# Kernel optimization log

Measured on AMD Instinct MI355X. Metric: run time of the kernel, lower is better.

Reference implementation:

```python
import jax, jax.numpy as jnp
import numpy as np


def setup_inputs() -> dict:
    key = jax.random.key(0)
    ks = jax.random.split(key, 8)
    B, Q, K, F, FV, C = 8, 2048, 2048, 512, 512, 2
    q = jax.random.normal(ks[0], (B, Q, F), dtype=jnp.float32)
    k = jax.random.normal(ks[1], (B, K, F), dtype=jnp.float32)
    v = jax.random.normal(ks[2], (B, K, FV), dtype=jnp.float32)
    coords_q = jax.random.uniform(ks[3], (B, Q, C), dtype=jnp.float32)
    coords_k = jax.random.uniform(ks[4], (B, K, C), dtype=jnp.float32)
    attn_mask = jax.random.randint(ks[5], (B, Q, K), 0, 2).astype(bool)
    alibi_mask = jax.random.randint(ks[6], (B, Q, K), 0, 2).astype(bool)
    bias_scale = jax.random.uniform(ks[7], (1,), dtype=jnp.float32)
    return {"q": q, "k": k, "v": v, "coords_q": coords_q, "coords_k": coords_k,
            "attn_mask": attn_mask, "alibi_mask": alibi_mask, "bias_scale": bias_scale}


def reference(q, k, v, coords_q, coords_k, attn_mask, alibi_mask, bias_scale):
    # scaled dot-product logits: [B, Q, K]
    scale = k.shape[-1] ** -0.5
    weight_logits = jnp.einsum('bqf,bkf->bqk', q, k) * scale
    # pairwise Euclidean coordinate distances: [B, Q, K]
    diff = coords_q[:, :, None, :] - coords_k[:, None, :, :]
    distances = jnp.linalg.norm(diff, axis=-1)
    # _RunningMeanScaler in eval mode divides by running_mean == 1 (identity)
    scaled_distances = distances * bias_scale  # bias_scale broadcasts from [1]
    scaled_distances = jnp.where(alibi_mask, 0.0, scaled_distances)
    weights = jax.nn.softmax(weight_logits, axis=-1)
    # post-softmax bias subtraction + masking (non-standard attention)
    weights = jnp.where(attn_mask, 0.0, weights - scaled_distances)
    attention = jnp.einsum('bqk,bkf->bqf', weights, v)
    return attention
```

## Files before the change

kernel.cpp:

```cpp
#include <hip/hip_runtime.h>
#include <hip/hip_bf16.h>
#include <math.h>

#define BN  8
#define QN  2048
#define KN  2048
#define FN  512
#define FVN 512

typedef __bf16 bf16x8 __attribute__((ext_vector_type(8)));
typedef __bf16 bf16x4v __attribute__((ext_vector_type(4)));
typedef float  f32x4  __attribute__((ext_vector_type(4)));

__device__ inline bf16x8 pack8(float4 a, float4 b) {
  bf16x8 r;
  r[0] = (__bf16)a.x; r[1] = (__bf16)a.y; r[2] = (__bf16)a.z; r[3] = (__bf16)a.w;
  r[4] = (__bf16)b.x; r[5] = (__bf16)b.y; r[6] = (__bf16)b.z; r[7] = (__bf16)b.w;
  return r;
}

__global__ __launch_bounds__(256) void gemm_s(
    const float* __restrict__ qm, const float* __restrict__ km,
    __bf16* __restrict__ Sws, int b0, int q0, int qchunk) {
  __shared__ __align__(16) __bf16 As[128][40];
  __shared__ __align__(16) __bf16 Bs[128][40];
  const int tid = threadIdx.x;
  const int lane = tid & 63, wave = tid >> 6;
  const int wq = (wave & 1) * 64, wk = (wave >> 1) * 64;
  const int qt = blockIdx.x * 128, kt = blockIdx.y * 128;
  const int z = blockIdx.z, b = b0 + z;
  __bf16* S = Sws + (size_t)z * qchunk * KN;
  const float* qbase = qm + ((size_t)b * QN + q0 + qt) * FN;
  const float* kbase = km + ((size_t)b * KN + kt) * FN;
  const int sr = tid >> 1;
  const int sc = (tid & 1) * 16;
  const int r = lane & 15, quad = lane >> 4;
  f32x4 acc[4][4] = {};
  for (int f0 = 0; f0 < FN; f0 += 32) {
    const float* qp = qbase + (size_t)sr * FN + f0 + sc;
    const float* kp = kbase + (size_t)sr * FN + f0 + sc;
    float4 a0 = *(const float4*)(qp);
    float4 a1 = *(const float4*)(qp + 4);
    float4 a2 = *(const float4*)(qp + 8);
    float4 a3 = *(const float4*)(qp + 12);
    float4 b0v = *(const float4*)(kp);
    float4 b1v = *(const float4*)(kp + 4);
    float4 b2v = *(const float4*)(kp + 8);
    float4 b3v = *(const float4*)(kp + 12);
    __syncthreads();
    *(bf16x8*)&As[sr][sc]     = pack8(a0, a1);
    *(bf16x8*)&As[sr][sc + 8] = pack8(a2, a3);
    *(bf16x8*)&Bs[sr][sc]     = pack8(b0v, b1v);
    *(bf16x8*)&Bs[sr][sc + 8] = pack8(b2v, b3v);
    __syncthreads();
    bf16x8 af[4], bf[4];
#pragma unroll
    for (int i = 0; i < 4; i++) af[i] = *(bf16x8*)&As[wq + i * 16 + r][quad * 8];
#pragma unroll
    for (int j = 0; j < 4; j++) bf[j] = *(bf16x8*)&Bs[wk + j * 16 + r][quad * 8];
#pragma unroll
    for (int i = 0; i < 4; i++)
#pragma unroll
      for (int j = 0; j < 4; j++)
        acc[i][j] = __builtin_amdgcn_mfma_f32_16x16x32_bf16(af[i], bf[j], acc[i][j], 0, 0, 0);
  }
  const float scale = 0.044194173824159216f;
#pragma unroll
  for (int i = 0; i < 4; i++)
#pragma unroll
    for (int j = 0; j < 4; j++)
#pragma unroll
      for (int t = 0; t < 4; t++) {
        int qq = qt + wq + i * 16 + quad * 4 + t;
        int kk = kt + wk + j * 16 + r;
        S[(size_t)qq * KN + kk] = (__bf16)(acc[i][j][t] * scale);
      }
}

__global__ __launch_bounds__(256) void softmax_w(
    __bf16* __restrict__ Sws,
    const float* __restrict__ cq, const float* __restrict__ ck,
    const int* __restrict__ attn, const int* __restrict__ alibi,
    const float* __restrict__ bsp, int b0, int q0, int qchunk) {
  const int z = blockIdx.z, b = b0 + z;
  const int ql = blockIdx.x;
  const int qg = q0 + ql;
  __bf16* Srow = Sws + ((size_t)z * qchunk + ql) * KN;
  const int tid = threadIdx.x;
  const int lane = tid & 63, wave = tid >> 6;
  const int k0 = tid * 8;
  bf16x8 s8 = *(bf16x8*)(Srow + k0);
  float sv[8];
#pragma unroll
  for (int i = 0; i < 8; i++) sv[i] = (float)s8[i];
  float m = sv[0];
#pragma unroll
  for (int i = 1; i < 8; i++) m = fmaxf(m, sv[i]);
  for (int o = 32; o > 0; o >>= 1) m = fmaxf(m, __shfl_xor(m, o));
  __shared__ float red[8];
  if (lane == 0) red[wave] = m;
  __syncthreads();
  m = fmaxf(fmaxf(red[0], red[1]), fmaxf(red[2], red[3]));
  float p[8];
  float s = 0.f;
#pragma unroll
  for (int i = 0; i < 8; i++) { p[i] = __expf(sv[i] - m); s += p[i]; }
  for (int o = 32; o > 0; o >>= 1) s += __shfl_xor(s, o);
  if (lane == 0) red[4 + wave] = s;
  __syncthreads();
  const float inv = 1.0f / (red[4] + red[5] + red[6] + red[7]);
  const int* arow = attn + ((size_t)b * QN + qg) * KN + k0;
  const int* lrow = alibi + ((size_t)b * QN + qg) * KN + k0;
  int4 am0 = *(const int4*)(arow);
  int4 am1 = *(const int4*)(arow + 4);
  int4 al0 = *(const int4*)(lrow);
  int4 al1 = *(const int4*)(lrow + 4);
  const float* ckb = ck + ((size_t)b * KN + k0) * 2;
  float4 c0 = *(const float4*)(ckb);
  float4 c1 = *(const float4*)(ckb + 4);
  float4 c2 = *(const float4*)(ckb + 8);
  float4 c3 = *(const float4*)(ckb + 12);
  const float qx = cq[((size_t)b * QN + qg) * 2 + 0];
  const float qy = cq[((size_t)b * QN + qg) * 2 + 1];
  const float bs = bsp[0];
  int   am[8] = {am0.x, am0.y, am0.z, am0.w, am1.x, am1.y, am1.z, am1.w};
  int   al[8] = {al0.x, al0.y, al0.z, al0.w, al1.x, al1.y, al1.z, al1.w};
  float kx[8] = {c0.x, c0.z, c1.x, c1.z, c2.x, c2.z, c3.x, c3.z};
  float ky[8] = {c0.y, c0.w, c1.y, c1.w, c2.y, c2.w, c3.y, c3.w};
  bf16x8 w8;
#pragma unroll
  for (int j = 0; j < 8; j++) {
    float dx = qx - kx[j], dy = qy - ky[j];
    float sd = al[j] ? 0.f : sqrtf(dx * dx + dy * dy) * bs;
    float w = am[j] ? 0.f : (p[j] * inv - sd);
    w8[j] = (__bf16)w;
  }
  *(bf16x8*)(Srow + k0) = w8;
}

__global__ __launch_bounds__(256) void transpose_v(
    const float* __restrict__ vm, __bf16* __restrict__ Vt, int b0) {
  const int z = blockIdx.z, b = b0 + z;
  const int k0 = blockIdx.x * 64, f0 = blockIdx.y * 64;
  __shared__ float tile[64][65];
  const int tid = threadIdx.x;
  const int r = tid >> 4;
  const int c = (tid & 15) * 4;
#pragma unroll
  for (int i = 0; i < 4; i++) {
    float4 u = *(const float4*)(vm + ((size_t)b * KN + k0 + r + i * 16) * FVN + f0 + c);
    tile[r + i * 16][c] = u.x; tile[r + i * 16][c + 1] = u.y;
    tile[r + i * 16][c + 2] = u.z; tile[r + i * 16][c + 3] = u.w;
  }
  __syncthreads();
#pragma unroll
  for (int i = 0; i < 4; i++) {
    int fv = r + i * 16;
    bf16x4v w;
    w[0] = (__bf16)tile[c][fv];     w[1] = (__bf16)tile[c + 1][fv];
    w[2] = (__bf16)tile[c + 2][fv]; w[3] = (__bf16)tile[c + 3][fv];
    *(bf16x4v*)(Vt + ((size_t)z * FVN + f0 + fv) * KN + k0 + c) = w;
  }
}

__global__ __launch_bounds__(256) void gemm_w(
    const __bf16* __restrict__ W, const __bf16* __restrict__ Vt,
    float* __restrict__ out, int b0, int q0, int qchunk) {
  __shared__ __align__(16) __bf16 As[128][40];
  __shared__ __align__(16) __bf16 Bs[128][40];
  const int tid = threadIdx.x;
  const int lane = tid & 63, wave = tid >> 6;
  const int wq = (wave & 1) * 64, wf = (wave >> 1) * 64;
  const int qt = blockIdx.x * 128, ft = blockIdx.y * 128;
  const int z = blockIdx.z, b = b0 + z;
  const __bf16* Wb = W + ((size_t)z * qchunk + qt) * KN;
  const __bf16* Vb = Vt + ((size_t)z * FVN + ft) * KN;
  const int sr = tid >> 1;
  const int sc = (tid & 1) * 16;
  const int r = lane & 15, quad = lane >> 4;
  f32x4 acc[4][4] = {};
  for (int k0 = 0; k0 < KN; k0 += 32) {
    bf16x8 a0 = *(const bf16x8*)(Wb + (size_t)sr * KN + k0 + sc);
    bf16x8 a1 = *(const bf16x8*)(Wb + (size_t)sr * KN + k0 + sc + 8);
    bf16x8 b0v = *(const bf16x8*)(Vb + (size_t)sr * KN + k0 + sc);
    bf16x8 b1v = *(const bf16x8*)(Vb + (size_t)sr * KN + k0 + sc + 8);
    __syncthreads();
    *(bf16x8*)&As[sr][sc]     = a0;
    *(bf16x8*)&As[sr][sc + 8] = a1;
    *(bf16x8*)&Bs[sr][sc]     = b0v;
    *(bf16x8*)&Bs[sr][sc + 8] = b1v;
    __syncthreads();
    bf16x8 af[4], bf[4];
#pragma unroll
    for (int i = 0; i < 4; i++) af[i] = *(bf16x8*)&As[wq + i * 16 + r][quad * 8];
#pragma unroll
    for (int j = 0; j < 4; j++) bf[j] = *(bf16x8*)&Bs[wf + j * 16 + r][quad * 8];
#pragma unroll
    for (int i = 0; i < 4; i++)
#pragma unroll
      for (int j = 0; j < 4; j++)
        acc[i][j] = __builtin_amdgcn_mfma_f32_16x16x32_bf16(af[i], bf[j], acc[i][j], 0, 0, 0);
  }
#pragma unroll
  for (int i = 0; i < 4; i++)
#pragma unroll
    for (int j = 0; j < 4; j++)
#pragma unroll
      for (int t = 0; t < 4; t++) {
        int qq = q0 + qt + wq + i * 16 + quad * 4 + t;
        int fv = ft + wf + j * 16 + r;
        out[((size_t)b * QN + qq) * FVN + fv] = acc[i][j][t];
      }
}

extern "C" void kernel_launch(void* const* d_in, const int* in_sizes, int n_in,
                              void* d_out, int out_size, void* d_ws, size_t ws_size,
                              hipStream_t stream) {
  (void)in_sizes; (void)n_in; (void)out_size;
  const float* qm   = (const float*)d_in[0];
  const float* km   = (const float*)d_in[1];
  const float* vm   = (const float*)d_in[2];
  const float* cq   = (const float*)d_in[3];
  const float* ck   = (const float*)d_in[4];
  const int*   attn = (const int*)d_in[5];
  const int*   alibi= (const int*)d_in[6];
  const float* bsp  = (const float*)d_in[7];
  float* out = (float*)d_out;

  auto need = [](int nb_, int qc_) -> size_t {
    return (size_t)nb_ * qc_ * KN * 2 + (size_t)nb_ * FVN * KN * 2;
  };
  int nb = BN, qc = QN;
  while (nb > 1 && need(nb, qc) > ws_size) nb >>= 1;
  while (qc > 128 && need(nb, qc) > ws_size) qc >>= 1;
  __bf16* Sws = (__bf16*)d_ws;
  __bf16* Vt  = (__bf16*)((char*)d_ws + (size_t)nb * qc * KN * 2);

  for (int b0 = 0; b0 < BN; b0 += nb) {
    transpose_v<<<dim3(KN / 64, FVN / 64, nb), 256, 0, stream>>>(vm, Vt, b0);
    for (int q0 = 0; q0 < QN; q0 += qc) {
      gemm_s<<<dim3(qc / 128, KN / 128, nb), 256, 0, stream>>>(qm, km, Sws, b0, q0, qc);
      softmax_w<<<dim3(qc, 1, nb), 256, 0, stream>>>(Sws, cq, ck, attn, alibi, bsp, b0, q0, qc);
      gemm_w<<<dim3(qc / 128, FVN / 128, nb), 256, 0, stream>>>(Sws, Vt, out, b0, q0, qc);
    }
  }
}
```

Measured before the change: 506.2 us.

## Pre-convert Q/K to bf16 and stage GEMM tiles via direct global-to-LDS loads

Adds a pre-pass that converts Q (with the softmax scale folded in) and K to bf16 once. Both GEMMs now stage tiles with global_load_lds 16-byte direct copies into unpadded LDS, which removes register round-trips and the per-tile fp32-to-bf16 conversion in gemm_s. V is transposed for all batches up front. The trade-offs are extra workspace, an additional conversion pass over Q/K, and the loss of LDS padding, which may cause bank conflicts on the fragment reads.

```diff
diff --git a/kernel.cpp b/kernel.cpp
--- a/kernel.cpp
+++ b/kernel.cpp
@@ -19,39 +19,54 @@
   return r;
 }
 
+__device__ __forceinline__ void g2l16(const __bf16* g, __bf16* l) {
+  __builtin_amdgcn_global_load_lds(
+      (const __attribute__((address_space(1))) void*)g,
+      (__attribute__((address_space(3))) void*)l,
+      16, 0, 0);
+}
+
+__global__ __launch_bounds__(256) void convert_qk(
+    const float* __restrict__ qm, const float* __restrict__ km,
+    __bf16* __restrict__ qb, __bf16* __restrict__ kb) {
+  const size_t idx = ((size_t)blockIdx.x * 256 + threadIdx.x) * 8;
+  const float scale = 0.044194173824159216f;
+  if (blockIdx.y == 0) {
+    float4 a = *(const float4*)(qm + idx);
+    float4 b = *(const float4*)(qm + idx + 4);
+    a.x *= scale; a.y *= scale; a.z *= scale; a.w *= scale;
+    b.x *= scale; b.y *= scale; b.z *= scale; b.w *= scale;
+    *(bf16x8*)(qb + idx) = pack8(a, b);
+  } else {
+    float4 a = *(const float4*)(km + idx);
+    float4 b = *(const float4*)(km + idx + 4);
+    *(bf16x8*)(kb + idx) = pack8(a, b);
+  }
+}
+
 __global__ __launch_bounds__(256) void gemm_s(
-    const float* __restrict__ qm, const float* __restrict__ km,
+    const __bf16* __restrict__ qb, const __bf16* __restrict__ kb,
     __bf16* __restrict__ Sws, int b0, int q0, int qchunk) {
-  __shared__ __align__(16) __bf16 As[128][40];
-  __shared__ __align__(16) __bf16 Bs[128][40];
+  __shared__ __align__(16) __bf16 As[128][32];
+  __shared__ __align__(16) __bf16 Bs[128][32];
   const int tid = threadIdx.x;
   const int lane = tid & 63, wave = tid >> 6;
   const int wq = (wave & 1) * 64, wk = (wave >> 1) * 64;
   const int qt = blockIdx.x * 128, kt = blockIdx.y * 128;
   const int z = blockIdx.z, b = b0 + z;
   __bf16* S = Sws + (size_t)z * qchunk * KN;
-  const float* qbase = qm + ((size_t)b * QN + q0 + qt) * FN;
-  const float* kbase = km + ((size_t)b * KN + kt) * FN;
-  const int sr = tid >> 1;
-  const int sc = (tid & 1) * 16;
+  const __bf16* Ab = qb + ((size_t)b * QN + q0 + qt) * FN;
+  const __bf16* Bb = kb + ((size_t)b * KN + kt) * FN;
+  const int srow = lane >> 2;
+  const int scol = (lane & 3) * 8;
   const int r = lane & 15, quad = lane >> 4;
   f32x4 acc[4][4] = {};
   for (int f0 = 0; f0 < FN; f0 += 32) {
-    const float* qp = qbase + (size_t)sr * FN + f0 + sc;
-    const float* kp = kbase + (size_t)sr * FN + f0 + sc;
-    float4 a0 = *(const float4*)(qp);
-    float4 a1 = *(const float4*)(qp + 4);
-    float4 a2 = *(const float4*)(qp + 8);
-    float4 a3 = *(const float4*)(qp + 12);
-    float4 b0v = *(const float4*)(kp);
-    float4 b1v = *(const float4*)(kp + 4);
-    float4 b2v = *(const float4*)(kp + 8);
-    float4 b3v = *(const float4*)(kp + 12);
-    __syncthreads();
-    *(bf16x8*)&As[sr][sc]     = pack8(a0, a1);
-    *(bf16x8*)&As[sr][sc + 8] = pack8(a2, a3);
-    *(bf16x8*)&Bs[sr][sc]     = pack8(b0v, b1v);
-    *(bf16x8*)&Bs[sr][sc + 8] = pack8(b2v, b3v);
+    __syncthreads();
+    g2l16(Ab + (size_t)(wave * 32 + srow) * FN + f0 + scol,      &As[wave * 32][0]);
+    g2l16(Ab + (size_t)(wave * 32 + 16 + srow) * FN + f0 + scol, &As[wave * 32 + 16][0]);
+    g2l16(Bb + (size_t)(wave * 32 + srow) * FN + f0 + scol,      &Bs[wave * 32][0]);
+    g2l16(Bb + (size_t)(wave * 32 + 16 + srow) * FN + f0 + scol, &Bs[wave * 32 + 16][0]);
     __syncthreads();
     bf16x8 af[4], bf[4];
 #pragma unroll
@@ -64,7 +79,6 @@
       for (int j = 0; j < 4; j++)
         acc[i][j] = __builtin_amdgcn_mfma_f32_16x16x32_bf16(af[i], bf[j], acc[i][j], 0, 0, 0);
   }
-  const float scale = 0.044194173824159216f;
 #pragma unroll
   for (int i = 0; i < 4; i++)
 #pragma unroll
@@ -73,7 +87,7 @@
       for (int t = 0; t < 4; t++) {
         int qq = qt + wq + i * 16 + quad * 4 + t;
         int kk = kt + wk + j * 16 + r;
-        S[(size_t)qq * KN + kk] = (__bf16)(acc[i][j][t] * scale);
+        S[(size_t)qq * KN + kk] = (__bf16)acc[i][j][t];
       }
 }
 
@@ -139,8 +153,8 @@
 }
 
 __global__ __launch_bounds__(256) void transpose_v(
-    const float* __restrict__ vm, __bf16* __restrict__ Vt, int b0) {
-  const int z = blockIdx.z, b = b0 + z;
+    const float* __restrict__ vm, __bf16* __restrict__ Vt) {
+  const int b = blockIdx.z;
   const int k0 = blockIdx.x * 64, f0 = blockIdx.y * 64;
   __shared__ float tile[64][65];
   const int tid = threadIdx.x;
@@ -159,36 +173,32 @@
     bf16x4v w;
     w[0] = (__bf16)tile[c][fv];     w[1] = (__bf16)tile[c + 1][fv];
     w[2] = (__bf16)tile[c + 2][fv]; w[3] = (__bf16)tile[c + 3][fv];
-    *(bf16x4v*)(Vt + ((size_t)z * FVN + f0 + fv) * KN + k0 + c) = w;
+    *(bf16x4v*)(Vt + ((size_t)b * FVN + f0 + fv) * KN + k0 + c) = w;
   }
 }
 
 __global__ __launch_bounds__(256) void gemm_w(
     const __bf16* __restrict__ W, const __bf16* __restrict__ Vt,
     float* __restrict__ out, int b0, int q0, int qchunk) {
-  __shared__ __align__(16) __bf16 As[128][40];
-  __shared__ __align__(16) __bf16 Bs[128][40];
+  __shared__ __align__(16) __bf16 As[128][32];
+  __shared__ __align__(16) __bf16 Bs[128][32];
   const int tid = threadIdx.x;
   const int lane = tid & 63, wave = tid >> 6;
   const int wq = (wave & 1) * 64, wf = (wave >> 1) * 64;
   const int qt = blockIdx.x * 128, ft = blockIdx.y * 128;
   const int z = blockIdx.z, b = b0 + z;
-  const __bf16* Wb = W + ((size_t)z * qchunk + qt) * KN;
-  const __bf16* Vb = Vt + ((size_t)z * FVN + ft) * KN;
-  const int sr = tid >> 1;
-  const int sc = (tid & 1) * 16;
+  const __bf16* Ab = W + ((size_t)z * qchunk + qt) * KN;
+  const __bf16* Bb = Vt + ((size_t)b * FVN + ft) * KN;
+  const int srow = lane >> 2;
+  const int scol = (lane & 3) * 8;
   const int r = lane & 15, quad = lane >> 4;
   f32x4 acc[4][4] = {};
   for (int k0 = 0; k0 < KN; k0 += 32) {
-    bf16x8 a0 = *(const bf16x8*)(Wb + (size_t)sr * KN + k0 + sc);
-    bf16x8 a1 = *(const bf16x8*)(Wb + (size_t)sr * KN + k0 + sc + 8);
-    bf16x8 b0v = *(const bf16x8*)(Vb + (size_t)sr * KN + k0 + sc);
-    bf16x8 b1v = *(const bf16x8*)(Vb + (size_t)sr * KN + k0 + sc + 8);
-    __syncthreads();
-    *(bf16x8*)&As[sr][sc]     = a0;
-    *(bf16x8*)&As[sr][sc + 8] = a1;
-    *(bf16x8*)&Bs[sr][sc]     = b0v;
-    *(bf16x8*)&Bs[sr][sc + 8] = b1v;
+    __syncthreads();
+    g2l16(Ab + (size_t)(wave * 32 + srow) * KN + k0 + scol,      &As[wave * 32][0]);
+    g2l16(Ab + (size_t)(wave * 32 + 16 + srow) * KN + k0 + scol, &As[wave * 32 + 16][0]);
+    g2l16(Bb + (size_t)(wave * 32 + srow) * KN + k0 + scol,      &Bs[wave * 32][0]);
+    g2l16(Bb + (size_t)(wave * 32 + 16 + srow) * KN + k0 + scol, &Bs[wave * 32 + 16][0]);
     __syncthreads();
     bf16x8 af[4], bf[4];
 #pragma unroll
@@ -227,19 +237,21 @@
   const float* bsp  = (const float*)d_in[7];
   float* out = (float*)d_out;
 
-  auto need = [](int nb_, int qc_) -> size_t {
-    return (size_t)nb_ * qc_ * KN * 2 + (size_t)nb_ * FVN * KN * 2;
-  };
+  __bf16* qb  = (__bf16*)d_ws;
+  __bf16* kb  = qb + (size_t)BN * QN * FN;
+  __bf16* Vt  = kb + (size_t)BN * KN * FN;
+  __bf16* Sws = Vt + (size_t)BN * FVN * KN;
+  const size_t fixed = ((size_t)BN * QN * FN + (size_t)BN * KN * FN +
+                        (size_t)BN * FVN * KN) * 2;
   int nb = BN, qc = QN;
-  while (nb > 1 && need(nb, qc) > ws_size) nb >>= 1;
-  while (qc > 128 && need(nb, qc) > ws_size) qc >>= 1;
-  __bf16* Sws = (__bf16*)d_ws;
-  __bf16* Vt  = (__bf16*)((char*)d_ws + (size_t)nb * qc * KN * 2);
-
+  while (nb > 1 && fixed + (size_t)nb * qc * KN * 2 > ws_size) nb >>= 1;
+  while (qc > 128 && fixed + (size_t)nb * qc * KN * 2 > ws_size) qc >>= 1;
+
+  convert_qk<<<dim3((BN * QN * FN) / 2048, 2), 256, 0, stream>>>(qm, km, qb, kb);
+  transpose_v<<<dim3(KN / 64, FVN / 64, BN), 256, 0, stream>>>(vm, Vt);
   for (int b0 = 0; b0 < BN; b0 += nb) {
-    transpose_v<<<dim3(KN / 64, FVN / 64, nb), 256, 0, stream>>>(vm, Vt, b0);
     for (int q0 = 0; q0 < QN; q0 += qc) {
-      gemm_s<<<dim3(qc / 128, KN / 128, nb), 256, 0, stream>>>(qm, km, Sws, b0, q0, qc);
+      gemm_s<<<dim3(qc / 128, KN / 128, nb), 256, 0, stream>>>(qb, kb, Sws, b0, q0, qc);
       softmax_w<<<dim3(qc, 1, nb), 256, 0, stream>>>(Sws, cq, ck, attn, alibi, bsp, b0, q0, qc);
       gemm_w<<<dim3(qc / 128, FVN / 128, nb), 256, 0, stream>>>(Sws, Vt, out, b0, q0, qc);
     }
```

After: 477.9 us. 5.6% less time.
